# Kernel tuning notes

Measured on AMD Instinct MI355X. Metric: run time of the kernel, lower is better.

The kernel has to match this reference:

```python
import jax, jax.numpy as jnp
import numpy as np

B, S, C = 2, 2048, 1024
U, H = 1024, 16
FFH = int(U * 4.0)
NEG = -1e9
EPS = 1e-5


def setup_inputs() -> dict:
    key = jax.random.key(0)
    ks = jax.random.split(key, 16)
    w = lambda k, sh: jax.random.normal(k, sh, dtype=jnp.float32) * 0.02
    return {
        'x': jax.random.normal(ks[0], (B, S, C), dtype=jnp.float32),
        'wq': w(ks[1], (C, U)), 'bq': jnp.zeros((U,), jnp.float32),
        'wk': w(ks[2], (C, U)), 'bk': jnp.zeros((U,), jnp.float32),
        'wv': w(ks[3], (C, U)), 'bv': jnp.zeros((U,), jnp.float32),
        'wf1': w(ks[4], (U, FFH)), 'bf1': jnp.zeros((FFH,), jnp.float32),
        'wf2': w(ks[5], (FFH, U)), 'bf2': jnp.zeros((U,), jnp.float32),
        'ln_g': jnp.ones((S, U), jnp.float32), 'ln_b': jnp.zeros((S, U), jnp.float32),
        'ffln_g': jnp.ones((S, U), jnp.float32), 'ffln_b': jnp.zeros((S, U), jnp.float32),
    }


def _ln2d(x, g, b):
    # LayerNorm over last two dims ([len_ts, units]) as in nn.LayerNorm([S, U])
    m = jnp.mean(x, axis=(-2, -1), keepdims=True)
    v = jnp.mean(jnp.square(x - m), axis=(-2, -1), keepdims=True)
    return (x - m) * jax.lax.rsqrt(v + EPS) * g + b


def reference(x, wq, bq, wk, bk, wv, bv, wf1, bf1, wf2, bf2, ln_g, ln_b, ffln_g, ffln_b):
    dh = U // H
    Q = (x @ wq + bq).reshape(B, S, H, dh)
    K = (x @ wk + bk).reshape(B, S, H, dh)
    V = (x @ wv + bv).reshape(B, S, H, dh)
    scores = jnp.einsum('bqhd,bkhd->bhqk', Q, K) / jnp.sqrt(jnp.float32(dh))
    mask = jnp.tril(jnp.ones((S, S), dtype=bool))  # causal tril buffer
    scores = jnp.where(mask, scores, NEG)
    attn = jax.nn.softmax(scores, axis=-1)
    out = jnp.einsum('bhqk,bkhd->bqhd', attn, V).reshape(B, S, U)
    out = out + x  # residual
    out = _ln2d(out, ln_g, ln_b)
    ff = jax.nn.relu(out @ wf1 + bf1) @ wf2 + bf2
    out = _ln2d(out + ff, ffln_g, ffln_b)
    return out
```

## Files before the change

### kernel.cpp

```cpp
#include <hip/hip_runtime.h>
#include <hip/hip_bf16.h>

typedef short s16x8 __attribute__((ext_vector_type(8)));
typedef float f32x4 __attribute__((ext_vector_type(4)));
typedef float f32x16 __attribute__((ext_vector_type(16)));
typedef unsigned short u16x4 __attribute__((ext_vector_type(4)));
typedef unsigned u32x4 __attribute__((ext_vector_type(4)));

#define DEV static __device__ __forceinline__

DEV unsigned short f2bf(float f) {
  __hip_bfloat16 h = __float2bfloat16(f);
  return *reinterpret_cast<unsigned short*>(&h);
}
DEV float bf2f(unsigned short u) {
  union { unsigned u; float f; } v; v.u = (unsigned)u << 16; return v.f;
}

#define GLDS16(src, dst) \
  __builtin_amdgcn_global_load_lds((const __attribute__((address_space(1))) void*)(src), \
                                   (__attribute__((address_space(3))) void*)(dst), 16, 0, 0)

#define MFMA(a, b, c) __builtin_amdgcn_mfma_f32_16x16x32_bf16((a), (b), (c), 0, 0, 0)
#define MFMA32(a, b, c) __builtin_amdgcn_mfma_f32_32x32x16_bf16((a), (b), (c), 0, 0, 0)

__global__ __launch_bounds__(256) void k_f32_to_bf16(const float* __restrict__ in,
                                                     unsigned short* __restrict__ out, int n4) {
  int i = blockIdx.x * 256 + threadIdx.x;
  if (i >= n4) return;
  float4 v = ((const float4*)in)[i];
  u16x4 o; o.x = f2bf(v.x); o.y = f2bf(v.y); o.z = f2bf(v.z); o.w = f2bf(v.w);
  ((u16x4*)out)[i] = o;
}

__global__ __launch_bounds__(256) void k_transpose_w(const float* __restrict__ W,
                                                     unsigned short* __restrict__ Wt,
                                                     int K, int N, float scale) {
  __shared__ float t[64][65];
  int k0 = blockIdx.x * 64, n0 = blockIdx.y * 64;
  int tid = threadIdx.x;
#pragma unroll
  for (int i = 0; i < 16; ++i) {
    int idx = tid + i * 256; int r = idx >> 6, c = idx & 63;
    t[r][c] = W[(size_t)(k0 + r) * N + (n0 + c)];
  }
  __syncthreads();
#pragma unroll
  for (int i = 0; i < 16; ++i) {
    int idx = tid + i * 256; int r = idx >> 6, c = idx & 63;
    Wt[(size_t)(n0 + r) * K + (k0 + c)] = f2bf(t[c][r] * scale);
  }
}

__global__ void k_concat3(const float* __restrict__ a, const float* __restrict__ b,
                          const float* __restrict__ c, float* __restrict__ out, int n, float sa) {
  int i = blockIdx.x * 256 + threadIdx.x;
  if (i >= 3 * n) return;
  int j = (i < n) ? i : (i < 2 * n ? i - n : i - 2 * n);
  out[i] = (i < n) ? a[j] * sa : (i < 2 * n ? b[j] : c[j]);
}

template <int MODE>
__global__ __launch_bounds__(512, 2) void k_gemm8(
    const unsigned short* __restrict__ A, int lda,
    const unsigned short* __restrict__ Bt, int ldb,
    const float* __restrict__ bias,
    unsigned short* __restrict__ Cb, float* __restrict__ Cf, int ldc,
    int K, int nnt, size_t zstride,
    unsigned short* __restrict__ Cq, unsigned short* __restrict__ Ck,
    unsigned short* __restrict__ Cv) {
  __shared__ __align__(16) unsigned short As[2 * 2 * 8192];
  __shared__ __align__(16) unsigned short Bs[2 * 2 * 8192];
  int nwg = gridDim.x;
  int bid = blockIdx.x;
  int cpx = nwg >> 3;
  int swz = (bid & 7) * cpx + (bid >> 3);
  int mt = swz / nnt, nt = swz % nnt;
  int m0 = mt * 256, n0 = nt * 256;
  int tid = threadIdx.x, w = tid >> 6, l = tid & 63;
  int wm = (w >> 2) * 128, wn = (w & 3) * 64;
  int kb = blockIdx.z * K;

  int sr = tid >> 2;
  int gsrc = (tid & 3) ^ ((sr >> 1) & 3);
  const unsigned short* Ag0 = A + (size_t)(m0 + sr) * lda + kb + gsrc * 8;
  const unsigned short* Ag1 = Ag0 + (size_t)128 * lda;
  const unsigned short* Bg0 = Bt + (size_t)(n0 + sr) * ldb + kb + gsrc * 8;
  const unsigned short* Bg1 = Bg0 + (size_t)128 * ldb;

#define STG_A(t, kh) do { int _c = (t) * 64 + (kh) * 32; int _d = ((((t) & 1) * 2 + (kh)) * 8192); \
    GLDS16(Ag0 + _c, &As[_d + tid * 8]); GLDS16(Ag1 + _c, &As[_d + 4096 + tid * 8]); } while (0)
#define STG_B(t, kh) do { int _c = (t) * 64 + (kh) * 32; int _d = ((((t) & 1) * 2 + (kh)) * 8192); \
    GLDS16(Bg0 + _c, &Bs[_d + tid * 8]); GLDS16(Bg1 + _c, &Bs[_d + 4096 + tid * 8]); } while (0)

  int lswz = (l >> 1) & 3;
  int acol = ((l >> 4) ^ lswz) * 8;
  const unsigned short* Afr = &As[(wm + (l & 15)) * 32 + acol];
  const unsigned short* Bfr = &Bs[(wn + (l & 15)) * 32 + acol];

  f32x4 acc[8][4] = {};
  int nkt = K >> 6;

  STG_A(0, 0); STG_B(0, 0); STG_A(0, 1); STG_B(0, 1); STG_A(1, 0); STG_B(1, 0);
  asm volatile("s_waitcnt vmcnt(4)" ::: "memory");
  __builtin_amdgcn_s_barrier();
  __builtin_amdgcn_sched_barrier(0);

  for (int t = 0; t < nkt; ++t) {
    int cur = t & 1, rem = nkt - t;
    const unsigned short* ab = Afr + cur * 16384;
    const unsigned short* bb = Bfr + cur * 16384;
    s16x8 af[4], bf[4];
    if (t + 1 < nkt) STG_A(t + 1, 1);
#pragma unroll
    for (int nr = 0; nr < 4; ++nr) bf[nr] = *(const s16x8*)(bb + nr * 512);
#pragma unroll
    for (int mr = 0; mr < 4; ++mr) af[mr] = *(const s16x8*)(ab + mr * 512);
    __builtin_amdgcn_s_setprio(1);
#pragma unroll
    for (int mr = 0; mr < 4; ++mr)
#pragma unroll
      for (int nr = 0; nr < 4; ++nr)
        acc[mr][nr] = MFMA(af[mr], bf[nr], acc[mr][nr]);
    __builtin_amdgcn_s_setprio(0);
    if (t + 1 < nkt) STG_B(t + 1, 1);
#pragma unroll
    for (int mr = 0; mr < 4; ++mr) af[mr] = *(const s16x8*)(ab + 2048 + mr * 512);
    __builtin_amdgcn_s_setprio(1);
#pragma unroll
    for (int mr = 0; mr < 4; ++mr)
#pragma unroll
      for (int nr = 0; nr < 4; ++nr)
        acc[mr + 4][nr] = MFMA(af[mr], bf[nr], acc[mr + 4][nr]);
    __builtin_amdgcn_s_setprio(0);
    if (rem >= 2) { asm volatile("s_waitcnt vmcnt(4)" ::: "memory"); }
    else          { asm volatile("s_waitcnt vmcnt(0)" ::: "memory"); }
    __builtin_amdgcn_s_barrier();
    __builtin_amdgcn_sched_barrier(0);
    if (t + 2 < nkt) STG_A(t + 2, 0);
#pragma unroll
    for (int nr = 0; nr < 4; ++nr) bf[nr] = *(const s16x8*)(bb + 8192 + nr * 512);
#pragma unroll
    for (int mr = 0; mr < 4; ++mr) af[mr] = *(const s16x8*)(ab + 8192 + mr * 512);
    __builtin_amdgcn_s_setprio(1);
#pragma unroll
    for (int mr = 0; mr < 4; ++mr)
#pragma unroll
      for (int nr = 0; nr < 4; ++nr)
        acc[mr][nr] = MFMA(af[mr], bf[nr], acc[mr][nr]);
    __builtin_amdgcn_s_setprio(0);
    if (t + 2 < nkt) STG_B(t + 2, 0);
#pragma unroll
    for (int mr = 0; mr < 4; ++mr) af[mr] = *(const s16x8*)(ab + 8192 + 2048 + mr * 512);
    __builtin_amdgcn_s_setprio(1);
#pragma unroll
    for (int mr = 0; mr < 4; ++mr)
#pragma unroll
      for (int nr = 0; nr < 4; ++nr)
        acc[mr + 4][nr] = MFMA(af[mr], bf[nr], acc[mr + 4][nr]);
    __builtin_amdgcn_s_setprio(0);
    if (rem >= 3) { asm volatile("s_waitcnt vmcnt(4)" ::: "memory"); }
    else          { asm volatile("s_waitcnt vmcnt(0)" ::: "memory"); }
    __builtin_amdgcn_s_barrier();
    __builtin_amdgcn_sched_barrier(0);
  }
#undef STG_A
#undef STG_B

  if (MODE == 4) {
    if (nt < 8) {
      unsigned short* dst = (nt < 4) ? Cq : Ck;
      int cb = (nt < 4) ? 0 : 1024;
#pragma unroll
      for (int mr = 0; mr < 8; ++mr) {
        int rb = m0 + wm + mr * 16 + (l >> 4) * 4;
#pragma unroll
        for (int nr = 0; nr < 4; ++nr) {
          int col = n0 + wn + nr * 16 + (l & 15);
          float bv = bias[col];
#pragma unroll
          for (int j = 0; j < 4; ++j)
            dst[(size_t)(rb + j) * 1024 + (col - cb)] = f2bf(acc[mr][nr][j] + bv);
        }
      }
    } else {
#pragma unroll
      for (int mr = 0; mr < 8; ++mr) {
        int rb = m0 + wm + mr * 16 + (l >> 4) * 4;
        int b2 = rb >> 11, s2 = rb & 2047;
        int s2p = (s2 & ~12) | ((s2 & 4) << 1) | ((s2 & 8) >> 1);
#pragma unroll
        for (int nr = 0; nr < 4; ++nr) {
          int col2 = n0 - 2048 + wn + nr * 16 + (l & 15);
          float bv = bias[col2 + 2048];
          u16x4 pk;
#pragma unroll
          for (int j = 0; j < 4; ++j) ((unsigned short*)&pk)[j] = f2bf(acc[mr][nr][j] + bv);
          *(u16x4*)(Cv + ((size_t)((b2 * 16 + (col2 >> 6)) * 64 + (col2 & 63))) * 2048 + s2p) = pk;
        }
      }
    }
    return;
  }
  unsigned short* Cbz = (MODE == 3) ? (Cb + zstride * blockIdx.z) : Cb;
#pragma unroll
  for (int mr = 0; mr < 8; ++mr) {
    int rb = m0 + wm + mr * 16 + (l >> 4) * 4;
#pragma unroll
    for (int nr = 0; nr < 4; ++nr) {
      int col = n0 + wn + nr * 16 + (l & 15);
      float bv = (MODE == 3) ? 0.f : bias[col];
#pragma unroll
      for (int j = 0; j < 4; ++j) {
        float v = acc[mr][nr][j] + bv;
        size_t off = (size_t)(rb + j) * ldc + col;
        if (MODE == 1) v = fmaxf(v, 0.f);
        Cbz[off] = f2bf(v);
      }
    }
  }
}

__global__ __launch_bounds__(256) void k_ff2_reduce(
    unsigned short* __restrict__ slices, const float* __restrict__ bias,
    const unsigned short* __restrict__ resid, float* __restrict__ partials) {
  __shared__ float red[8];
  int i = blockIdx.x;
  size_t rb = (size_t)i * 4096;
  int c = threadIdx.x * 4;
  u16x4 a0 = *(const u16x4*)(slices + rb + c);
  u16x4 a1 = *(const u16x4*)(slices + rb + 1024 + c);
  u16x4 a2 = *(const u16x4*)(slices + rb + 2048 + c);
  u16x4 a3 = *(const u16x4*)(slices + rb + 3072 + c);
  float4 bv = *(const float4*)(bias + c);
  u16x4 rv = *(const u16x4*)(resid + (size_t)i * 1024 + c);
  float4 o;
  o.x = bf2f(a0.x) + bf2f(a1.x) + bf2f(a2.x) + bf2f(a3.x) + bv.x + bf2f(rv.x);
  o.y = bf2f(a0.y) + bf2f(a1.y) + bf2f(a2.y) + bf2f(a3.y) + bv.y + bf2f(rv.y);
  o.z = bf2f(a0.z) + bf2f(a1.z) + bf2f(a2.z) + bf2f(a3.z) + bv.z + bf2f(rv.z);
  o.w = bf2f(a0.w) + bf2f(a1.w) + bf2f(a2.w) + bf2f(a3.w) + bv.w + bf2f(rv.w);
  __syncthreads();
  *(float4*)((float*)slices + (size_t)i * 2048 + c) = o;
  float bsum = o.x + o.y + o.z + o.w;
  float bsq = o.x * o.x + o.y * o.y + o.z * o.z + o.w * o.w;
  int wv = threadIdx.x >> 6, lv = threadIdx.x & 63;
#pragma unroll
  for (int mk = 1; mk < 64; mk <<= 1) { bsum += __shfl_xor(bsum, mk); bsq += __shfl_xor(bsq, mk); }
  if (lv == 0) { red[wv] = bsum; red[4 + wv] = bsq; }
  __syncthreads();
  if (threadIdx.x == 0) {
    partials[i * 2] = red[0] + red[1] + red[2] + red[3];
    partials[i * 2 + 1] = red[4] + red[5] + red[6] + red[7];
  }
}

__global__ __launch_bounds__(128, 2) void k_attn(
    const unsigned short* __restrict__ Qg, const unsigned short* __restrict__ Kg,
    const unsigned short* __restrict__ Vt,
    const float* __restrict__ x, unsigned short* __restrict__ hpre,
    float* __restrict__ partials, int S, int H) {
  __shared__ __align__(16) unsigned short Ks[2][4096];
  __shared__ __align__(16) unsigned short Vs[2][4096];
  __shared__ float ascr[2][32];
  __shared__ float red[4];
  int bh = blockIdx.x, b = bh >> 4, h = bh & 15;
  const int nqt = S / 64;
  int qt = nqt - 1 - (int)blockIdx.y;
  int tid = threadIdx.x, w = tid >> 6, l = tid & 63;
  int lo = l & 31, hi5 = l >> 5;
  const int U = H * 64;
  const unsigned short* Qb = Qg + (size_t)(b * S) * 1024 + h * 64;
  const unsigned short* Kb = Kg + (size_t)(b * S) * 1024 + h * 64;
  const unsigned short* Vb = Vt + (size_t)bh * 64 * S;

  int sg_r[4], sg_c[4];
#pragma unroll
  for (int it = 0; it < 4; ++it) {
    int g = it * 128 + tid;
    sg_r[it] = g >> 3;
    sg_c[it] = ((g & 7) ^ ((g >> 3) & 7)) * 8;
  }
  int qrow = qt * 64 + w * 32 + lo;
  s16x8 qf[4];
#pragma unroll
  for (int s = 0; s < 4; ++s)
    qf[s] = *(const s16x8*)(Qb + (size_t)qrow * 1024 + s * 16 + hi5 * 8);

  int krow[16];
#pragma unroll
  for (int r = 0; r < 16; ++r) krow[r] = (r & 3) + 8 * (r >> 2) + 4 * hi5;

  f32x16 o0 = {}, o1 = {};
  float m = -1e30f, lsum = 0.f;

#pragma unroll
  for (int it = 0; it < 4; ++it) {
    GLDS16(Kb + (size_t)sg_r[it] * 1024 + sg_c[it], &Ks[0][(it * 128 + tid) * 8]);
    GLDS16(Vb + (size_t)sg_r[it] * S + sg_c[it], &Vs[0][(it * 128 + tid) * 8]);
  }

  for (int kt = 0; kt <= qt; ++kt) {
    int cur = kt & 1;
    __syncthreads();
    if (kt < qt) {
      int nb = cur ^ 1, kn = (kt + 1) * 64;
#pragma unroll
      for (int it = 0; it < 4; ++it) {
        GLDS16(Kb + (size_t)(kn + sg_r[it]) * 1024 + sg_c[it], &Ks[nb][(it * 128 + tid) * 8]);
        GLDS16(Vb + (size_t)sg_r[it] * S + kn + sg_c[it], &Vs[nb][(it * 128 + tid) * 8]);
      }
    }
    f32x16 sc0 = {}, sc1 = {};
    __builtin_amdgcn_s_setprio(1);
#pragma unroll
    for (int s = 0; s < 4; ++s) {
      int gc = ((2 * s + hi5) ^ (lo & 7)) * 8;
      s16x8 kf0 = *(const s16x8*)&Ks[cur][lo * 64 + gc];
      s16x8 kf1 = *(const s16x8*)&Ks[cur][(32 + lo) * 64 + gc];
      sc0 = MFMA32(kf0, qf[s], sc0);
      sc1 = MFMA32(kf1, qf[s], sc1);
    }
    __builtin_amdgcn_s_setprio(0);
    if (kt == qt) {
      int wq = w * 32 + lo;
#pragma unroll
      for (int r = 0; r < 16; ++r) {
        if (krow[r] > wq) sc0[r] = -1e30f;
        if (krow[r] + 32 > wq) sc1[r] = -1e30f;
      }
    }
    float mx = sc0[0];
#pragma unroll
    for (int r = 1; r < 16; ++r) mx = fmaxf(mx, sc0[r]);
#pragma unroll
    for (int r = 0; r < 16; ++r) mx = fmaxf(mx, sc1[r]);
    mx = fmaxf(mx, __shfl_xor(mx, 32));
    if (__ballot(mx > m + 11.5415603f)) {
      float mnew = fmaxf(m, mx);
      float alpha = __builtin_amdgcn_exp2f(m - mnew);
      m = mnew;
      lsum *= alpha;
      if (l < 32) ascr[w][lo] = alpha;
#pragma unroll
      for (int r = 0; r < 16; ++r) {
        float aj = ascr[w][krow[r]];
        o0[r] *= aj; o1[r] *= aj;
      }
    }
    float rs = 0.f;
    unsigned wk0[8], wk1[8];
#pragma unroll
    for (int j = 0; j < 8; ++j) {
      float p0 = __builtin_amdgcn_exp2f(sc0[2 * j] - m);
      float p1 = __builtin_amdgcn_exp2f(sc0[2 * j + 1] - m);
      rs += p0 + p1;
      wk0[j] = (unsigned)f2bf(p0) | ((unsigned)f2bf(p1) << 16);
      float p2 = __builtin_amdgcn_exp2f(sc1[2 * j] - m);
      float p3 = __builtin_amdgcn_exp2f(sc1[2 * j + 1] - m);
      rs += p2 + p3;
      wk1[j] = (unsigned)f2bf(p2) | ((unsigned)f2bf(p3) << 16);
    }
    rs += __shfl_xor(rs, 32);
    lsum += rs;
    __builtin_amdgcn_s_setprio(1);
#pragma unroll
    for (int s = 0; s < 4; ++s) {
      u32x4 paw;
      if (s == 0)      { paw.x = wk0[0]; paw.y = wk0[1]; paw.z = wk0[2]; paw.w = wk0[3]; }
      else if (s == 1) { paw.x = wk0[4]; paw.y = wk0[5]; paw.z = wk0[6]; paw.w = wk0[7]; }
      else if (s == 2) { paw.x = wk1[0]; paw.y = wk1[1]; paw.z = wk1[2]; paw.w = wk1[3]; }
      else             { paw.x = wk1[4]; paw.y = wk1[5]; paw.z = wk1[6]; paw.w = wk1[7]; }
      s16x8 pa = *(s16x8*)&paw;
      int gc = ((2 * s + hi5) ^ (lo & 7)) * 8;
      s16x8 vf0 = *(const s16x8*)&Vs[cur][lo * 64 + gc];
      s16x8 vf1 = *(const s16x8*)&Vs[cur][(32 + lo) * 64 + gc];
      o0 = MFMA32(pa, vf0, o0);
      o1 = MFMA32(pa, vf1, o1);
    }
    __builtin_amdgcn_s_setprio(0);
  }
  if (l < 32) ascr[w][lo] = 1.f / lsum;
  float bsum = 0.f, bsq = 0.f;
  unsigned short* hb = hpre + (size_t)(b * S) * U + h * 64;
  const float* xb = x + (size_t)(b * S) * U + h * 64;
#pragma unroll
  for (int r = 0; r < 16; ++r) {
    float inv = ascr[w][krow[r]];
    int srow = qt * 64 + w * 32 + krow[r];
    size_t base = (size_t)srow * U + lo;
    float v0 = o0[r] * inv + xb[base];
    float v1 = o1[r] * inv + xb[base + 32];
    hb[base] = f2bf(v0);
    hb[base + 32] = f2bf(v1);
    bsum += v0 + v1; bsq += v0 * v0 + v1 * v1;
  }
#pragma unroll
  for (int mk = 1; mk < 64; mk <<= 1) { bsum += __shfl_xor(bsum, mk); bsq += __shfl_xor(bsq, mk); }
  if (l == 0) { red[w * 2] = bsum; red[w * 2 + 1] = bsq; }
  __syncthreads();
  if (tid == 0) {
    int pi = b * (H * nqt) + h * nqt + qt;
    partials[pi * 2] = red[0] + red[2];
    partials[pi * 2 + 1] = red[1] + red[3];
  }
}

__global__ __launch_bounds__(256) void k_ln_stats(const float* __restrict__ partials, int nper,
                                                  float* __restrict__ stats, float invN) {
  int b = blockIdx.x, tid = threadIdx.x;
  float s = 0.f, q = 0.f;
  for (int i = tid; i < nper; i += 256) { s += partials[(b * nper + i) * 2]; q += partials[(b * nper + i) * 2 + 1]; }
#pragma unroll
  for (int mk = 1; mk < 64; mk <<= 1) { s += __shfl_xor(s, mk); q += __shfl_xor(q, mk); }
  __shared__ float red[8];
  int w = tid >> 6, l = tid & 63;
  if (l == 0) { red[w] = s; red[4 + w] = q; }
  __syncthreads();
  if (tid == 0) {
    s = red[0] + red[1] + red[2] + red[3];
    q = red[4] + red[5] + red[6] + red[7];
    float m = s * invN, var = q * invN - m * m;
    stats[b * 2] = m; stats[b * 2 + 1] = rsqrtf(var + 1e-5f);
  }
}

__global__ __launch_bounds__(256) void k_ln_apply_b(
    const unsigned short* __restrict__ src, const float* __restrict__ stats,
    const float* __restrict__ g, const float* __restrict__ bt,
    unsigned short* __restrict__ outb, int SU) {
  int b = blockIdx.y;
  int idx = (blockIdx.x * 256 + threadIdx.x) * 4;
  float m = stats[b * 2], r = stats[b * 2 + 1];
  u16x4 v4 = *(const u16x4*)(src + (size_t)b * SU + idx);
  float4 gg = *(const float4*)(g + idx);
  float4 bb = *(const float4*)(bt + idx);
  u16x4 ob;
  ob.x = f2bf((bf2f(v4.x) - m) * r * gg.x + bb.x);
  ob.y = f2bf((bf2f(v4.y) - m) * r * gg.y + bb.y);
  ob.z = f2bf((bf2f(v4.z) - m) * r * gg.z + bb.z);
  ob.w = f2bf((bf2f(v4.w) - m) * r * gg.w + bb.w);
  *(u16x4*)(outb + (size_t)b * SU + idx) = ob;
}

__global__ __launch_bounds__(256) void k_ln_apply2(
    const float* __restrict__ src, const float* __restrict__ stats,
    const float* __restrict__ g, const float* __restrict__ bt,
    float* __restrict__ outf) {
  int b = blockIdx.y;
  int row = blockIdx.x;
  int grow = b * 2048 + row;
  int c = threadIdx.x * 4;
  float m = stats[b * 2], r = stats[b * 2 + 1];
  float4 v = *(const float4*)(src + (size_t)grow * 2048 + c);
  float4 gg = *(const float4*)(g + (size_t)row * 1024 + c);
  float4 bb = *(const float4*)(bt + (size_t)row * 1024 + c);
  float4 o;
  o.x = (v.x - m) * r * gg.x + bb.x;
  o.y = (v.y - m) * r * gg.y + bb.y;
  o.z = (v.z - m) * r * gg.z + bb.z;
  o.w = (v.w - m) * r * gg.w + bb.w;
  *(float4*)(outf + (size_t)grow * 1024 + c) = o;
}

extern "C" void kernel_launch(void* const* d_in, const int* in_sizes, int n_in,
                              void* d_out, int out_size, void* d_ws, size_t ws_size,
                              hipStream_t stream) {
  (void)in_sizes; (void)n_in; (void)out_size; (void)ws_size;
  const int S = 2048, H = 16;
  const float* x   = (const float*)d_in[0];
  const float* wq  = (const float*)d_in[1];
  const float* bq  = (const float*)d_in[2];
  const float* wk  = (const float*)d_in[3];
  const float* bk  = (const float*)d_in[4];
  const float* wv  = (const float*)d_in[5];
  const float* bv  = (const float*)d_in[6];
  const float* wf1 = (const float*)d_in[7];
  const float* bf1 = (const float*)d_in[8];
  const float* wf2 = (const float*)d_in[9];
  const float* bf2 = (const float*)d_in[10];
  const float* lng = (const float*)d_in[11];
  const float* lnb = (const float*)d_in[12];
  const float* ffg = (const float*)d_in[13];
  const float* ffb = (const float*)d_in[14];

  char* ws = (char*)d_ws;
  unsigned short* wqkvT = (unsigned short*)(ws);
  unsigned short* wf1T  = (unsigned short*)(ws + 6291456);
  unsigned short* wf2T  = (unsigned short*)(ws + 14680064);
  unsigned short* xb    = (unsigned short*)(ws + 23068672);
  unsigned short* qb    = (unsigned short*)(ws + 31457280);
  unsigned short* kbuf  = (unsigned short*)(ws + 39845888);
  unsigned short* vt    = (unsigned short*)(ws + 56623104);
  unsigned short* h1b   = (unsigned short*)(ws + 65011712);
  unsigned short* hpreb = (unsigned short*)(ws + 73400320);
  unsigned short* ff2s  = (unsigned short*)(ws + 73400320);
  unsigned short* f1b   = (unsigned short*)(ws + 23068672);
  float* biasqkv        = (float*)(ws + 106954752);
  float* part_attn      = (float*)(ws + 106967040);
  float* stats1         = (float*)(ws + 106977280);
  float* ffpart2        = (float*)(ws);
  float* stats2         = (float*)(ws + 65536);

  const float qscale = 0.125f * 1.44269504f;
  k_f32_to_bf16<<<4096, 256, 0, stream>>>(x, xb, 4096 * 1024 / 4);
  k_transpose_w<<<dim3(16, 16), 256, 0, stream>>>(wq, wqkvT, 1024, 1024, qscale);
  k_transpose_w<<<dim3(16, 16), 256, 0, stream>>>(wk, wqkvT + 1024 * 1024, 1024, 1024, 1.0f);
  k_transpose_w<<<dim3(16, 16), 256, 0, stream>>>(wv, wqkvT + 2048 * 1024, 1024, 1024, 1.0f);
  k_transpose_w<<<dim3(16, 64), 256, 0, stream>>>(wf1, wf1T, 1024, 4096, 1.0f);
  k_transpose_w<<<dim3(64, 16), 256, 0, stream>>>(wf2, wf2T, 4096, 1024, 1.0f);
  k_concat3<<<12, 256, 0, stream>>>(bq, bk, bv, biasqkv, 1024, qscale);

  k_gemm8<4><<<dim3(192, 1, 1), 512, 0, stream>>>(xb, 1024, wqkvT, 1024, biasqkv,
      nullptr, nullptr, 0, 1024, 12, 0, qb, kbuf, vt);

  k_attn<<<dim3(32, 32), 128, 0, stream>>>(qb, kbuf, vt, x, hpreb, part_attn, S, H);

  k_ln_stats<<<2, 256, 0, stream>>>(part_attn, 512, stats1, 1.f / (2048.f * 1024.f));
  k_ln_apply_b<<<dim3(2048, 2), 256, 0, stream>>>(hpreb, stats1, lng, lnb, h1b, S * 1024);

  k_gemm8<1><<<dim3(256, 1, 1), 512, 0, stream>>>(h1b, 1024, wf1T, 1024, bf1,
      f1b, nullptr, 4096, 1024, 16, 0, nullptr, nullptr, nullptr);

  k_gemm8<3><<<dim3(64, 1, 4), 512, 0, stream>>>(f1b, 4096, wf2T, 4096, nullptr,
      ff2s, nullptr, 4096, 1024, 4, 1024, nullptr, nullptr, nullptr);

  k_ff2_reduce<<<4096, 256, 0, stream>>>(ff2s, bf2, h1b, ffpart2);

  k_ln_stats<<<2, 256, 0, stream>>>(ffpart2, 2048, stats2, 1.f / (2048.f * 1024.f));
  k_ln_apply2<<<dim3(2048, 2), 256, 0, stream>>>((float*)ff2s, stats2, ffg, ffb, (float*)d_out);
}
```

Measured before the change: 236.4 us.

## Give each wave private K/V LDS tiles with per-wave staging and waitcnt sync

Each wave in the causal attention kernel now loads its own full 64-row K and V tiles into a private LDS buffer, replacing the block-shared double buffer. This drops the per-iteration __syncthreads in favour of explicit vmcnt/lgkmcnt waits, and the next K tile is issued right after the QK MFMAs, the next V tile right after the PV MFMAs. The goal is to remove block-level barriers and let the two waves run independently. In exchange each block issues twice the global-to-LDS traffic for K/V and loses double buffering, so load latency is only partly hidden behind softmax work.

```diff
diff --git a/kernel.cpp b/kernel.cpp
--- a/kernel.cpp
+++ b/kernel.cpp
@@ -273,13 +273,17 @@
   const unsigned short* Kb = Kg + (size_t)(b * S) * 1024 + h * 64;
   const unsigned short* Vb = Vt + (size_t)bh * 64 * S;
 
-  int sg_r[4], sg_c[4];
-#pragma unroll
-  for (int it = 0; it < 4; ++it) {
-    int g = it * 128 + tid;
-    sg_r[it] = g >> 3;
-    sg_c[it] = ((g & 7) ^ ((g >> 3) & 7)) * 8;
-  }
+  int sr8 = l >> 3;
+  int sc8 = ((l & 7) ^ (sr8 & 7)) * 8;
+  unsigned short* KsW = &Ks[w][0];
+  unsigned short* VsW = &Vs[w][0];
+#define STG_K(kt) do { int _kn = (kt) * 64; \
+    _Pragma("unroll") for (int i2 = 0; i2 < 8; ++i2) \
+      GLDS16(Kb + (size_t)(_kn + i2 * 8 + sr8) * 1024 + sc8, KsW + i2 * 512 + l * 8); } while (0)
+#define STG_V(kt) do { int _kn = (kt) * 64; \
+    _Pragma("unroll") for (int i2 = 0; i2 < 8; ++i2) \
+      GLDS16(Vb + (size_t)(i2 * 8 + sr8) * S + _kn + sc8, VsW + i2 * 512 + l * 8); } while (0)
+
   int qrow = qt * 64 + w * 32 + lo;
   s16x8 qf[4];
 #pragma unroll
@@ -293,34 +297,25 @@
   f32x16 o0 = {}, o1 = {};
   float m = -1e30f, lsum = 0.f;
 
-#pragma unroll
-  for (int it = 0; it < 4; ++it) {
-    GLDS16(Kb + (size_t)sg_r[it] * 1024 + sg_c[it], &Ks[0][(it * 128 + tid) * 8]);
-    GLDS16(Vb + (size_t)sg_r[it] * S + sg_c[it], &Vs[0][(it * 128 + tid) * 8]);
-  }
+  STG_K(0); STG_V(0);
 
   for (int kt = 0; kt <= qt; ++kt) {
-    int cur = kt & 1;
-    __syncthreads();
-    if (kt < qt) {
-      int nb = cur ^ 1, kn = (kt + 1) * 64;
-#pragma unroll
-      for (int it = 0; it < 4; ++it) {
-        GLDS16(Kb + (size_t)(kn + sg_r[it]) * 1024 + sg_c[it], &Ks[nb][(it * 128 + tid) * 8]);
-        GLDS16(Vb + (size_t)sg_r[it] * S + kn + sg_c[it], &Vs[nb][(it * 128 + tid) * 8]);
-      }
-    }
+    asm volatile("s_waitcnt vmcnt(8)" ::: "memory");
+    __builtin_amdgcn_sched_barrier(0);
     f32x16 sc0 = {}, sc1 = {};
     __builtin_amdgcn_s_setprio(1);
 #pragma unroll
     for (int s = 0; s < 4; ++s) {
       int gc = ((2 * s + hi5) ^ (lo & 7)) * 8;
-      s16x8 kf0 = *(const s16x8*)&Ks[cur][lo * 64 + gc];
-      s16x8 kf1 = *(const s16x8*)&Ks[cur][(32 + lo) * 64 + gc];
+      s16x8 kf0 = *(const s16x8*)&KsW[lo * 64 + gc];
+      s16x8 kf1 = *(const s16x8*)&KsW[(32 + lo) * 64 + gc];
       sc0 = MFMA32(kf0, qf[s], sc0);
       sc1 = MFMA32(kf1, qf[s], sc1);
     }
     __builtin_amdgcn_s_setprio(0);
+    asm volatile("s_waitcnt lgkmcnt(0)" ::: "memory");
+    __builtin_amdgcn_sched_barrier(0);
+    if (kt < qt) STG_K(kt + 1);
     if (kt == qt) {
       int wq = w * 32 + lo;
 #pragma unroll
@@ -362,6 +357,9 @@
     }
     rs += __shfl_xor(rs, 32);
     lsum += rs;
+    if (kt < qt) { asm volatile("s_waitcnt vmcnt(8)" ::: "memory"); }
+    else         { asm volatile("s_waitcnt vmcnt(0)" ::: "memory"); }
+    __builtin_amdgcn_sched_barrier(0);
     __builtin_amdgcn_s_setprio(1);
 #pragma unroll
     for (int s = 0; s < 4; ++s) {
@@ -372,12 +370,15 @@
       else             { paw.x = wk1[4]; paw.y = wk1[5]; paw.z = wk1[6]; paw.w = wk1[7]; }
       s16x8 pa = *(s16x8*)&paw;
       int gc = ((2 * s + hi5) ^ (lo & 7)) * 8;
-      s16x8 vf0 = *(const s16x8*)&Vs[cur][lo * 64 + gc];
-      s16x8 vf1 = *(const s16x8*)&Vs[cur][(32 + lo) * 64 + gc];
+      s16x8 vf0 = *(const s16x8*)&VsW[lo * 64 + gc];
+      s16x8 vf1 = *(const s16x8*)&VsW[(32 + lo) * 64 + gc];
       o0 = MFMA32(pa, vf0, o0);
       o1 = MFMA32(pa, vf1, o1);
     }
     __builtin_amdgcn_s_setprio(0);
+    asm volatile("s_waitcnt lgkmcnt(0)" ::: "memory");
+    __builtin_amdgcn_sched_barrier(0);
+    if (kt < qt) STG_V(kt + 1);
   }
   if (l < 32) ascr[w][lo] = 1.f / lsum;
   float bsum = 0.f, bsq = 0.f;
@@ -403,6 +404,8 @@
     partials[pi * 2] = red[0] + red[2];
     partials[pi * 2 + 1] = red[1] + red[3];
   }
+#undef STG_K
+#undef STG_V
 }
 
 __global__ __launch_bounds__(256) void k_ln_stats(const float* __restrict__ partials, int nper,
```

New measurement: 240.5 us. No clear change (+1.7%).
